# Performance work log

Hardware: AMD Instinct MI355X
Metric: run time of the kernel (lower is better)

Reference implementation:

```python
import jax, jax.numpy as jnp
import numpy as np

B, T, U, D, V = 8, 128, 64, 512, 1024

def setup_inputs() -> dict:
    key = jax.random.key(0)
    k1, k2, k3, k4, k5, k6 = jax.random.split(key, 6)
    source_encodings = jax.random.normal(k1, (B, T, D), dtype=jnp.float32)
    target_encodings = jax.random.normal(k2, (B, U, D), dtype=jnp.float32)
    source_lengths = jax.random.randint(k3, (B,), 1, T + 1, dtype=jnp.int32)
    target_lengths = jax.random.randint(k4, (B,), 1, U + 1, dtype=jnp.int32)
    # Linear(D, V): weight (V, D), bias (V), init like torch default (uniform)
    bound = 1.0 / np.sqrt(D)
    W = jax.random.uniform(k5, (V, D), minval=-bound, maxval=bound, dtype=jnp.float32)
    b = jax.random.uniform(k6, (V,), minval=-bound, maxval=bound, dtype=jnp.float32)
    return {"source_encodings": source_encodings, "source_lengths": source_lengths,
            "target_encodings": target_encodings, "target_lengths": target_lengths,
            "W": W, "b": b}

def reference(source_encodings, source_lengths, target_encodings, target_lengths, W, b):
    # broadcast add: (B,T,1,D) + (B,1,U,D) -> (B,T,U,D)
    joint = source_encodings[:, :, None, :] + target_encodings[:, None, :, :]
    relu_out = jax.nn.relu(joint)
    # linear projection: (B,T,U,D) x (D,V) + b -> (B,T,U,V)
    output = jnp.einsum('btud,vd->btuv', relu_out, W) + b
    return (output, source_lengths, target_lengths)
```

## Files before the change

kernel.cpp:

```cpp
#include <hip/hip_runtime.h>

typedef unsigned short u16;
typedef float  f32x4  __attribute__((ext_vector_type(4)));
typedef int    i32x4  __attribute__((ext_vector_type(4)));
typedef __bf16 bf16x8 __attribute__((ext_vector_type(8)));

#define AS1 __attribute__((address_space(1)))
#define AS3 __attribute__((address_space(3)))

__device__ __forceinline__ void gload_lds16(const void* g, void* l) {
  __builtin_amdgcn_global_load_lds((AS1 void*)g, (AS3 void*)l, 16, 0, 0);
}

constexpr int B_ = 8, T_ = 128, U_ = 64, D_ = 512, V_ = 1024;
constexpr int M_ = B_ * T_ * U_;

__global__ void prep_w(const float* __restrict__ W,
                       const int* __restrict__ sl, const int* __restrict__ tl,
                       u16* __restrict__ Wb, float* __restrict__ tail) {
  if (blockIdx.x == 0 && threadIdx.x < 16) {
    const int t = threadIdx.x;
    tail[t] = (t < 8) ? (float)sl[t] : (float)tl[t - 8];
  }
  const int tid = blockIdx.x * 256 + threadIdx.x;
  const int v  = tid >> 6;
  const int cs = tid & 63;
  const float* sp = W + (size_t)v * D_ + cs * 8;
  float4 w0 = *(const float4*)sp;
  float4 w1 = *(const float4*)(sp + 4);
  union { __bf16 h[8]; i32x4 x; } pk;
  pk.h[0] = (__bf16)w0.x; pk.h[1] = (__bf16)w0.y;
  pk.h[2] = (__bf16)w0.z; pk.h[3] = (__bf16)w0.w;
  pk.h[4] = (__bf16)w1.x; pk.h[5] = (__bf16)w1.y;
  pk.h[6] = (__bf16)w1.z; pk.h[7] = (__bf16)w1.w;
  const int dc = (cs >> 3) * 8 + ((cs & 7) ^ (v & 7));
  *(i32x4*)(Wb + (size_t)v * D_ + dc * 8) = pk.x;
}

__global__ void tail_k(const int* __restrict__ sl, const int* __restrict__ tl,
                       float* __restrict__ tail) {
  const int t = threadIdx.x;
  if (t < 8)       tail[t] = (float)sl[t];
  else if (t < 16) tail[t] = (float)tl[t - 8];
}

__global__ __launch_bounds__(256, 3) void joiner_gemm(
    const float* __restrict__ src, const float* __restrict__ tgt,
    const u16* __restrict__ Wb, const float* __restrict__ bias,
    float* __restrict__ out)
{
  __shared__ __align__(16) char As[16384];
  __shared__ __align__(16) char Bs[2][16384];

  const int tid  = threadIdx.x;
  const int lane = tid & 63;
  const int wid  = tid >> 6;
  const int bn   = blockIdx.x & 7;
  const int bm   = blockIdx.x >> 3;
  const int bt0  = bm * 2;
  const int bb   = bt0 >> 7;
  const int sr0  = tid >> 3;
  const int sc8  = tid & 7;
  const int wm   = (wid >> 1) * 64;
  const int wn   = (wid & 1) * 64;

  f32x4 acc[4][4] = {};

  const float* srcp0 = src + (size_t)bt0 * D_ + sc8 * 8;
  const float* srcp1 = srcp0 + D_;
  const float* tgtp0 = tgt + ((size_t)bb * U_ + sr0) * D_ + sc8 * 8;
  const float* tgtp1 = tgtp0 + (size_t)32 * D_;

  float bv[4];
  #pragma unroll
  for (int ni = 0; ni < 4; ++ni)
    bv[ni] = bias[bn * 128 + wn + ni * 16 + (lane & 15)];

  const u16* bbase[4];
  #pragma unroll
  for (int q = 0; q < 4; ++q) {
    const int i   = wid * 4 + q;
    const int row = i * 8 + (lane >> 3);
    bbase[q] = Wb + (size_t)(bn * 128 + row) * D_ + (lane & 7) * 8;
  }

  float4 pS0a, pS0b, pS1a, pS1b, pT0a, pT0b, pT1a, pT1b;

  auto loadA = [&](int kt) {
    const int k0 = kt * 64;
    pS0a = *(const float4*)(srcp0 + k0); pS0b = *(const float4*)(srcp0 + k0 + 4);
    pS1a = *(const float4*)(srcp1 + k0); pS1b = *(const float4*)(srcp1 + k0 + 4);
    pT0a = *(const float4*)(tgtp0 + k0); pT0b = *(const float4*)(tgtp0 + k0 + 4);
    pT1a = *(const float4*)(tgtp1 + k0); pT1b = *(const float4*)(tgtp1 + k0 + 4);
  };
  auto issueB = [&](int kt, int nb) {
    #pragma unroll
    for (int q = 0; q < 4; ++q)
      gload_lds16(bbase[q] + kt * 64, Bs[nb] + (wid * 4 + q) * 1024);
  };

  auto expandA = [&]() {
    #pragma unroll
    for (int i = 0; i < 2; ++i) {
      const float4 sa = i ? pS1a : pS0a;
      const float4 sb = i ? pS1b : pS0b;
      #pragma unroll
      for (int j = 0; j < 2; ++j) {
        const float4 ta = j ? pT1a : pT0a;
        const float4 tb = j ? pT1b : pT0b;
        const int r = i * 64 + j * 32 + sr0;
        union { __bf16 h[8]; i32x4 x; } pk;
        pk.h[0] = (__bf16)fmaxf(sa.x + ta.x, 0.f);
        pk.h[1] = (__bf16)fmaxf(sa.y + ta.y, 0.f);
        pk.h[2] = (__bf16)fmaxf(sa.z + ta.z, 0.f);
        pk.h[3] = (__bf16)fmaxf(sa.w + ta.w, 0.f);
        pk.h[4] = (__bf16)fmaxf(sb.x + tb.x, 0.f);
        pk.h[5] = (__bf16)fmaxf(sb.y + tb.y, 0.f);
        pk.h[6] = (__bf16)fmaxf(sb.z + tb.z, 0.f);
        pk.h[7] = (__bf16)fmaxf(sb.w + tb.w, 0.f);
        *(i32x4*)(As + r * 128 + ((sc8 ^ (r & 7)) << 4)) = pk.x;
      }
    }
  };

  auto compute = [&](int cb) {
    #pragma unroll
    for (int s = 0; s < 2; ++s) {
      const int kc = s * 4 + (lane >> 4);
      bf16x8 af[4], bg[4];
      #pragma unroll
      for (int mi = 0; mi < 4; ++mi) {
        const int r = wm + mi * 16 + (lane & 15);
        af[mi] = *(const bf16x8*)(As + r * 128 + ((kc ^ (r & 7)) << 4));
      }
      #pragma unroll
      for (int ni = 0; ni < 4; ++ni) {
        const int n = wn + ni * 16 + (lane & 15);
        bg[ni] = *(const bf16x8*)(Bs[cb] + n * 128 + ((kc ^ (n & 7)) << 4));
      }
      __builtin_amdgcn_s_setprio(1);
      #pragma unroll
      for (int mi = 0; mi < 4; ++mi)
        #pragma unroll
        for (int ni = 0; ni < 4; ++ni)
          acc[mi][ni] = __builtin_amdgcn_mfma_f32_16x16x32_bf16(
              af[mi], bg[ni], acc[mi][ni], 0, 0, 0);
      __builtin_amdgcn_s_setprio(0);
    }
  };

  loadA(0);
  issueB(0, 0);
  expandA();
  asm volatile("s_waitcnt vmcnt(0) lgkmcnt(0)" ::: "memory");
  __builtin_amdgcn_sched_barrier(0);
  __builtin_amdgcn_s_barrier();
  __builtin_amdgcn_sched_barrier(0);

  for (int kt = 0; kt < 8; ++kt) {
    if (kt < 7) {
      loadA(kt + 1);
      issueB(kt + 1, (kt + 1) & 1);
    }
    __builtin_amdgcn_sched_barrier(0);
    compute(kt & 1);
    if (kt < 7) {
      __builtin_amdgcn_sched_barrier(0);
      __builtin_amdgcn_s_barrier();
      expandA();
      asm volatile("s_waitcnt vmcnt(0) lgkmcnt(0)" ::: "memory");
      __builtin_amdgcn_sched_barrier(0);
      __builtin_amdgcn_s_barrier();
      __builtin_amdgcn_sched_barrier(0);
    }
  }

  const int col = lane & 15;
  const int r4  = (lane >> 4) * 4;
  #pragma unroll
  for (int mi = 0; mi < 4; ++mi) {
    const size_t mrow = (size_t)bm * 128 + wm + mi * 16 + r4;
    float* op0 = out + mrow * V_ + bn * 128 + wn + col;
    #pragma unroll
    for (int ni = 0; ni < 4; ++ni) {
      float* op = op0 + ni * 16;
      const f32x4 v = acc[mi][ni];
      op[0 * V_] = v[0] + bv[ni];
      op[1 * V_] = v[1] + bv[ni];
      op[2 * V_] = v[2] + bv[ni];
      op[3 * V_] = v[3] + bv[ni];
    }
  }
}

__global__ __launch_bounds__(256, 2) void joiner_gemm_f32(
    const float* __restrict__ src, const float* __restrict__ tgt,
    const float* __restrict__ Wf, const float* __restrict__ bias,
    float* __restrict__ out)
{
  __shared__ char As[128 * 128];
  __shared__ char Bs[128 * 128];

  const int tid  = threadIdx.x;
  const int lane = tid & 63;
  const int wid  = tid >> 6;
  const int bn   = blockIdx.x & 7;
  const int bm   = blockIdx.x >> 3;
  const int bt0  = bm * 2;
  const int bb   = bt0 >> 7;
  const int sr0  = tid >> 3;
  const int sc8  = tid & 7;
  const int wm   = (wid >> 1) * 64;
  const int wn   = (wid & 1) * 64;

  f32x4 acc[4][4] = {};

  const float* srcp0 = src + (size_t)bt0 * D_ + sc8 * 8;
  const float* srcp1 = srcp0 + D_;
  const float* tgtp0 = tgt + ((size_t)bb * U_ + sr0) * D_ + sc8 * 8;
  const float* tgtp1 = tgtp0 + (size_t)32 * D_;

  for (int kt = 0; kt < 8; ++kt) {
    const int k0 = kt * 64;
    #pragma unroll
    for (int jj = 0; jj < 4; ++jj) {
      const int vr = sr0 + 32 * jj;
      const float* wp = Wf + (size_t)(bn * 128 + vr) * D_ + k0 + sc8 * 8;
      float4 w0 = *(const float4*)wp;
      float4 w1 = *(const float4*)(wp + 4);
      union { __bf16 h[8]; i32x4 x; } pk;
      pk.h[0] = (__bf16)w0.x; pk.h[1] = (__bf16)w0.y;
      pk.h[2] = (__bf16)w0.z; pk.h[3] = (__bf16)w0.w;
      pk.h[4] = (__bf16)w1.x; pk.h[5] = (__bf16)w1.y;
      pk.h[6] = (__bf16)w1.z; pk.h[7] = (__bf16)w1.w;
      *(i32x4*)(Bs + vr * 128 + ((sc8 ^ (vr & 7)) << 4)) = pk.x;
    }
    float4 s0a = *(const float4*)(srcp0 + k0), s0b = *(const float4*)(srcp0 + k0 + 4);
    float4 s1a = *(const float4*)(srcp1 + k0), s1b = *(const float4*)(srcp1 + k0 + 4);
    float4 t0a = *(const float4*)(tgtp0 + k0), t0b = *(const float4*)(tgtp0 + k0 + 4);
    float4 t1a = *(const float4*)(tgtp1 + k0), t1b = *(const float4*)(tgtp1 + k0 + 4);
    #pragma unroll
    for (int i = 0; i < 2; ++i) {
      const float4 sa = i ? s1a : s0a;
      const float4 sb = i ? s1b : s0b;
      #pragma unroll
      for (int jj = 0; jj < 2; ++jj) {
        const float4 ta = jj ? t1a : t0a;
        const float4 tb = jj ? t1b : t0b;
        const int r = i * 64 + jj * 32 + sr0;
        union { __bf16 h[8]; i32x4 x; } pk;
        pk.h[0] = (__bf16)fmaxf(sa.x + ta.x, 0.f);
        pk.h[1] = (__bf16)fmaxf(sa.y + ta.y, 0.f);
        pk.h[2] = (__bf16)fmaxf(sa.z + ta.z, 0.f);
        pk.h[3] = (__bf16)fmaxf(sa.w + ta.w, 0.f);
        pk.h[4] = (__bf16)fmaxf(sb.x + tb.x, 0.f);
        pk.h[5] = (__bf16)fmaxf(sb.y + tb.y, 0.f);
        pk.h[6] = (__bf16)fmaxf(sb.z + tb.z, 0.f);
        pk.h[7] = (__bf16)fmaxf(sb.w + tb.w, 0.f);
        *(i32x4*)(As + r * 128 + ((sc8 ^ (r & 7)) << 4)) = pk.x;
      }
    }
    __syncthreads();
    #pragma unroll
    for (int s = 0; s < 2; ++s) {
      const int kc = s * 4 + (lane >> 4);
      bf16x8 af[4], bg[4];
      #pragma unroll
      for (int mi = 0; mi < 4; ++mi) {
        const int r = wm + mi * 16 + (lane & 15);
        af[mi] = *(const bf16x8*)(As + r * 128 + ((kc ^ (r & 7)) << 4));
      }
      #pragma unroll
      for (int ni = 0; ni < 4; ++ni) {
        const int n = wn + ni * 16 + (lane & 15);
        bg[ni] = *(const bf16x8*)(Bs + n * 128 + ((kc ^ (n & 7)) << 4));
      }
      #pragma unroll
      for (int mi = 0; mi < 4; ++mi)
        #pragma unroll
        for (int ni = 0; ni < 4; ++ni)
          acc[mi][ni] = __builtin_amdgcn_mfma_f32_16x16x32_bf16(
              af[mi], bg[ni], acc[mi][ni], 0, 0, 0);
    }
    __syncthreads();
  }

  const int col = lane & 15;
  const int r4  = (lane >> 4) * 4;
  float bv[4];
  #pragma unroll
  for (int ni = 0; ni < 4; ++ni) bv[ni] = bias[bn * 128 + wn + ni * 16 + col];
  #pragma unroll
  for (int mi = 0; mi < 4; ++mi) {
    const size_t mrow = (size_t)bm * 128 + wm + mi * 16 + r4;
    float* op0 = out + mrow * V_ + bn * 128 + wn + col;
    #pragma unroll
    for (int ni = 0; ni < 4; ++ni) {
      float* op = op0 + ni * 16;
      const f32x4 v = acc[mi][ni];
      op[0 * V_] = v[0] + bv[ni];
      op[1 * V_] = v[1] + bv[ni];
      op[2 * V_] = v[2] + bv[ni];
      op[3 * V_] = v[3] + bv[ni];
    }
  }
}

extern "C" void kernel_launch(void* const* d_in, const int* in_sizes, int n_in,
                              void* d_out, int out_size, void* d_ws, size_t ws_size,
                              hipStream_t stream) {
  const float* src  = (const float*)d_in[0];
  const int*   sl   = (const int*)d_in[1];
  const float* tgt  = (const float*)d_in[2];
  const int*   tl   = (const int*)d_in[3];
  const float* W    = (const float*)d_in[4];
  const float* bias = (const float*)d_in[5];
  float* out  = (float*)d_out;
  float* tail = out + (size_t)M_ * V_;

  if (ws_size >= (size_t)V_ * D_ * sizeof(u16)) {
    u16* Wb = (u16*)d_ws;
    prep_w<<<256, 256, 0, stream>>>(W, sl, tl, Wb, tail);
    joiner_gemm<<<(M_ / 128) * (V_ / 128), 256, 0, stream>>>(
        src, tgt, Wb, bias, out);
  } else {
    tail_k<<<1, 64, 0, stream>>>(sl, tl, tail);
    joiner_gemm_f32<<<(M_ / 128) * (V_ / 128), 256, 0, stream>>>(
        src, tgt, W, bias, out);
  }
}
```

Baseline: 105.1 us.

## Prepack W into MFMA fragment order and load B fragments directly to registers

```diff
diff --git a/kernel.cpp b/kernel.cpp
--- a/kernel.cpp
+++ b/kernel.cpp
@@ -8,16 +8,12 @@
 #define AS1 __attribute__((address_space(1)))
 #define AS3 __attribute__((address_space(3)))
 
-__device__ __forceinline__ void gload_lds16(const void* g, void* l) {
-  __builtin_amdgcn_global_load_lds((AS1 void*)g, (AS3 void*)l, 16, 0, 0);
-}
-
 constexpr int B_ = 8, T_ = 128, U_ = 64, D_ = 512, V_ = 1024;
 constexpr int M_ = B_ * T_ * U_;
 
 __global__ void prep_w(const float* __restrict__ W,
                        const int* __restrict__ sl, const int* __restrict__ tl,
-                       u16* __restrict__ Wb, float* __restrict__ tail) {
+                       u16* __restrict__ Wb2, float* __restrict__ tail) {
   if (blockIdx.x == 0 && threadIdx.x < 16) {
     const int t = threadIdx.x;
     tail[t] = (t < 8) ? (float)sl[t] : (float)tl[t - 8];
@@ -33,8 +29,9 @@
   pk.h[2] = (__bf16)w0.z; pk.h[3] = (__bf16)w0.w;
   pk.h[4] = (__bf16)w1.x; pk.h[5] = (__bf16)w1.y;
   pk.h[6] = (__bf16)w1.z; pk.h[7] = (__bf16)w1.w;
-  const int dc = (cs >> 3) * 8 + ((cs & 7) ^ (v & 7));
-  *(i32x4*)(Wb + (size_t)v * D_ + dc * 8) = pk.x;
+  const int vg = v >> 4, vc = v & 15;
+  const int kc = cs >> 2, ko = cs & 3;
+  *(i32x4*)(Wb2 + (((size_t)(vg * 16 + kc) * 64 + ko * 16 + vc) * 8)) = pk.x;
 }
 
 __global__ void tail_k(const int* __restrict__ sl, const int* __restrict__ tl,
@@ -46,11 +43,10 @@
 
 __global__ __launch_bounds__(256, 3) void joiner_gemm(
     const float* __restrict__ src, const float* __restrict__ tgt,
-    const u16* __restrict__ Wb, const float* __restrict__ bias,
+    const u16* __restrict__ Wb2, const float* __restrict__ bias,
     float* __restrict__ out)
 {
   __shared__ __align__(16) char As[16384];
-  __shared__ __align__(16) char Bs[2][16384];
 
   const int tid  = threadIdx.x;
   const int lane = tid & 63;
@@ -76,15 +72,15 @@
   for (int ni = 0; ni < 4; ++ni)
     bv[ni] = bias[bn * 128 + wn + ni * 16 + (lane & 15)];
 
-  const u16* bbase[4];
-  #pragma unroll
-  for (int q = 0; q < 4; ++q) {
-    const int i   = wid * 4 + q;
-    const int row = i * 8 + (lane >> 3);
-    bbase[q] = Wb + (size_t)(bn * 128 + row) * D_ + (lane & 7) * 8;
+  const u16* bfr[4];
+  #pragma unroll
+  for (int ni = 0; ni < 4; ++ni) {
+    const int vg = bn * 8 + (wn >> 4) + ni;
+    bfr[ni] = Wb2 + ((size_t)vg * 16 * 64 + lane) * 8;
   }
 
   float4 pS0a, pS0b, pS1a, pS1b, pT0a, pT0b, pT1a, pT1b;
+  bf16x8 bg[4][2];
 
   auto loadA = [&](int kt) {
     const int k0 = kt * 64;
@@ -93,10 +89,13 @@
     pT0a = *(const float4*)(tgtp0 + k0); pT0b = *(const float4*)(tgtp0 + k0 + 4);
     pT1a = *(const float4*)(tgtp1 + k0); pT1b = *(const float4*)(tgtp1 + k0 + 4);
   };
-  auto issueB = [&](int kt, int nb) {
-    #pragma unroll
-    for (int q = 0; q < 4; ++q)
-      gload_lds16(bbase[q] + kt * 64, Bs[nb] + (wid * 4 + q) * 1024);
+
+  auto loadBg = [&](int kt) {
+    #pragma unroll
+    for (int ni = 0; ni < 4; ++ni)
+      #pragma unroll
+      for (int s = 0; s < 2; ++s)
+        bg[ni][s] = *(const bf16x8*)(bfr[ni] + (size_t)(kt * 2 + s) * 512);
   };
 
   auto expandA = [&]() {
@@ -123,20 +122,15 @@
     }
   };
 
-  auto compute = [&](int cb) {
+  auto compute = [&]() {
     #pragma unroll
     for (int s = 0; s < 2; ++s) {
       const int kc = s * 4 + (lane >> 4);
-      bf16x8 af[4], bg[4];
+      bf16x8 af[4];
       #pragma unroll
       for (int mi = 0; mi < 4; ++mi) {
         const int r = wm + mi * 16 + (lane & 15);
         af[mi] = *(const bf16x8*)(As + r * 128 + ((kc ^ (r & 7)) << 4));
-      }
-      #pragma unroll
-      for (int ni = 0; ni < 4; ++ni) {
-        const int n = wn + ni * 16 + (lane & 15);
-        bg[ni] = *(const bf16x8*)(Bs[cb] + n * 128 + ((kc ^ (n & 7)) << 4));
       }
       __builtin_amdgcn_s_setprio(1);
       #pragma unroll
@@ -144,31 +138,30 @@
         #pragma unroll
         for (int ni = 0; ni < 4; ++ni)
           acc[mi][ni] = __builtin_amdgcn_mfma_f32_16x16x32_bf16(
-              af[mi], bg[ni], acc[mi][ni], 0, 0, 0);
+              af[mi], bg[ni][s], acc[mi][ni], 0, 0, 0);
       __builtin_amdgcn_s_setprio(0);
     }
   };
 
   loadA(0);
-  issueB(0, 0);
   expandA();
-  asm volatile("s_waitcnt vmcnt(0) lgkmcnt(0)" ::: "memory");
+  loadBg(0);
+  asm volatile("s_waitcnt lgkmcnt(0)" ::: "memory");
   __builtin_amdgcn_sched_barrier(0);
   __builtin_amdgcn_s_barrier();
   __builtin_amdgcn_sched_barrier(0);
 
   for (int kt = 0; kt < 8; ++kt) {
+    if (kt < 7) loadA(kt + 1);
+    __builtin_amdgcn_sched_barrier(0);
+    compute();
+    __builtin_amdgcn_sched_barrier(0);
+    __builtin_amdgcn_s_barrier();
+    __builtin_amdgcn_sched_barrier(0);
     if (kt < 7) {
-      loadA(kt + 1);
-      issueB(kt + 1, (kt + 1) & 1);
-    }
-    __builtin_amdgcn_sched_barrier(0);
-    compute(kt & 1);
-    if (kt < 7) {
-      __builtin_amdgcn_sched_barrier(0);
-      __builtin_amdgcn_s_barrier();
+      loadBg(kt + 1);
       expandA();
-      asm volatile("s_waitcnt vmcnt(0) lgkmcnt(0)" ::: "memory");
+      asm volatile("s_waitcnt lgkmcnt(0)" ::: "memory");
       __builtin_amdgcn_sched_barrier(0);
       __builtin_amdgcn_s_barrier();
       __builtin_amdgcn_sched_barrier(0);
@@ -319,10 +312,10 @@
   float* tail = out + (size_t)M_ * V_;
 
   if (ws_size >= (size_t)V_ * D_ * sizeof(u16)) {
-    u16* Wb = (u16*)d_ws;
-    prep_w<<<256, 256, 0, stream>>>(W, sl, tl, Wb, tail);
+    u16* Wb2 = (u16*)d_ws;
+    prep_w<<<256, 256, 0, stream>>>(W, sl, tl, Wb2, tail);
     joiner_gemm<<<(M_ / 128) * (V_ / 128), 256, 0, stream>>>(
-        src, tgt, Wb, bias, out);
+        src, tgt, Wb2, bias, out);
   } else {
     tail_k<<<1, 64, 0, stream>>>(sl, tl, tail);
     joiner_gemm_f32<<<(M_ / 128) * (V_ / 128), 256, 0, stream>>>(
```

Result: no change. 103.4 us (-1.7%).
